# Kernel optimization log

Measured on AMD Instinct MI355X. Metric: run time of the kernel, lower is better.

The kernel has to match this reference:

```python
import jax, jax.numpy as jnp
from jax import lax
import numpy as np

SCALE = 1.0   # self.scale
EPS = 1e-12
CHUNK = 512   # points processed per chunk to bound [P,T,3] temporaries


def _closest_sqdist(p, a, b, c):
    """Squared distance from points p:[P,3] to triangles (a,b,c):[T,3] -> [P,T].
    Ericson's closest-point-on-triangle, fully vectorized."""
    ab = b - a
    ac = c - a
    bc = c - b
    ap = p[:, None, :] - a[None, :, :]
    bp = p[:, None, :] - b[None, :, :]
    cp = p[:, None, :] - c[None, :, :]
    d1 = jnp.einsum('td,ptd->pt', ab, ap)
    d2 = jnp.einsum('td,ptd->pt', ac, ap)
    d3 = jnp.einsum('td,ptd->pt', ab, bp)
    d4 = jnp.einsum('td,ptd->pt', ac, bp)
    d5 = jnp.einsum('td,ptd->pt', ab, cp)
    d6 = jnp.einsum('td,ptd->pt', ac, cp)
    va = d3 * d6 - d5 * d4
    vb = d5 * d2 - d1 * d6
    vc = d1 * d4 - d3 * d2

    def sdiv(n, d):  # NaN/Inf-safe division (branch is masked out by where anyway)
        return n / jnp.where(jnp.abs(d) < EPS, 1.0, d)

    t_ab = sdiv(d1, d1 - d3)[..., None]
    t_ac = sdiv(d2, d2 - d6)[..., None]
    t_bc = sdiv(d4 - d3, (d4 - d3) + (d5 - d6))[..., None]
    denom = va + vb + vc
    v_in = sdiv(vb, denom)[..., None]
    w_in = sdiv(vc, denom)[..., None]

    # base case: interior of the face; then overwrite with edge / vertex regions
    cl = a[None] + v_in * ab[None] + w_in * ac[None]
    cl = jnp.where(((va <= 0) & (d4 - d3 >= 0) & (d5 - d6 >= 0))[..., None],
                   b[None] + t_bc * bc[None], cl)   # edge BC
    cl = jnp.where(((vb <= 0) & (d2 >= 0) & (d6 <= 0))[..., None],
                   a[None] + t_ac * ac[None], cl)   # edge AC
    cl = jnp.where(((vc <= 0) & (d1 >= 0) & (d3 <= 0))[..., None],
                   a[None] + t_ab * ab[None], cl)   # edge AB
    cl = jnp.where(((d6 >= 0) & (d5 <= d6))[..., None], c[None], cl)  # vertex C
    cl = jnp.where(((d3 >= 0) & (d4 <= d3))[..., None], b[None], cl)  # vertex B
    cl = jnp.where(((d1 <= 0) & (d2 <= 0))[..., None], a[None], cl)   # vertex A
    diff = p[:, None, :] - cl
    return jnp.sum(diff * diff, axis=-1)


def setup_inputs():
    key = jax.random.key(0)
    k1, k2, k3 = jax.random.split(key, 3)
    vertices = jax.random.normal(k1, (4, 3, 16, 16, 16), dtype=jnp.float32)
    pc = jax.random.uniform(k2, (4, 4096, 3), dtype=jnp.float32)
    faces = jax.random.randint(k3, (8192, 3), 0, 4096, dtype=jnp.int32)
    return {"vertices": vertices, "pc": pc, "faces": faces}


def reference(vertices, pc, faces):
    B = vertices.shape[0]
    v = jax.nn.sigmoid(vertices)                     # self.normalization
    pos = jnp.moveaxis(v, 1, -1).reshape(B, -1, 3)   # permute(1,2,3,0).view(-1,3)
    pts = pc * SCALE                                 # _scale_points
    # pymesh path drops all-zero points; emulate with a mask (scaling keeps zeros zero)
    mask = jnp.any(pc != 0.0, axis=-1).astype(pts.dtype)  # [B,N]

    def per_batch(args):
        posb, pb, mb = args
        a = posb[faces[:, 0]]
        b = posb[faces[:, 1]]
        c = posb[faces[:, 2]]
        n_chunks = pb.shape[0] // CHUNK

        def chunk_min(pch):  # [CHUNK,3] -> [CHUNK] nearest sq-dist over all tris
            return jnp.min(_closest_sqdist(pch, a, b, c), axis=-1)

        d = lax.map(chunk_min, pb.reshape(n_chunks, CHUNK, 3)).reshape(-1)
        cnt = jnp.maximum(jnp.sum(mb), 1.0)
        return jnp.sum(d * mb) / cnt                 # mean(squared_distances)

    losses = lax.map(per_batch, (pos, pts, mask))    # [B]
    return jnp.mean(losses)
```

## Files before the change

### kernel.cpp

```cpp
#include <hip/hip_runtime.h>
#include <math.h>
#include <float.h>

#define NB 4
#define NP 4096
#define NT 8192
#define NS 64
#define TCH (NT/NS)
#define TREC 20
#define EPSD 1e-12

typedef float f2 __attribute__((ext_vector_type(2)));

__device__ __forceinline__ float sigm(float x) { return 1.0f / (1.0f + expf(-x)); }
__device__ __forceinline__ f2 vmin2(f2 a, f2 b) { return __builtin_elementwise_min(a, b); }
__device__ __forceinline__ f2 vmax2(f2 a, f2 b) { return __builtin_elementwise_max(a, b); }
__device__ __forceinline__ f2 clamp01(f2 x) {
  f2 z; z.x = 0.0f; z.y = 0.0f;
  f2 o; o.x = 1.0f; o.y = 1.0f;
  return vmin2(vmax2(x, z), o);
}

__global__ __launch_bounds__(256) void prep_kernel(
    const float* __restrict__ verts, const int* __restrict__ faces,
    float* __restrict__ tri)
{
  int idx = blockIdx.x * 256 + threadIdx.x;
  if (idx >= NB * NT) return;
  int b = idx >> 13;
  int t = idx & (NT - 1);
  int f0 = faces[3 * t + 0], f1 = faces[3 * t + 1], f2i = faces[3 * t + 2];
  const float* vb = verts + (size_t)b * 3 * NP;
  float ax = sigm(vb[f0]),  ay = sigm(vb[NP + f0]),  az = sigm(vb[2 * NP + f0]);
  float bx = sigm(vb[f1]),  by = sigm(vb[NP + f1]),  bz = sigm(vb[2 * NP + f1]);
  float cx = sigm(vb[f2i]), cy = sigm(vb[NP + f2i]), cz = sigm(vb[2 * NP + f2i]);
  float abx = bx - ax, aby = by - ay, abz = bz - az;
  float acx = cx - ax, acy = cy - ay, acz = cz - az;
  double aa = (double)abx * abx + (double)aby * aby + (double)abz * abz;
  double am = (double)abx * acx + (double)aby * acy + (double)abz * acz;
  double cc = (double)acx * acx + (double)acy * acy + (double)acz * acz;
  double den = aa * cc - am * am;
  double bb  = aa - 2.0 * am + cc;
  float raa  = (fabs(aa)  < EPSD) ? 1.0f : (float)(1.0 / aa);
  float rcc  = (fabs(cc)  < EPSD) ? 1.0f : (float)(1.0 / cc);
  float rbb  = (fabs(bb)  < EPSD) ? 1.0f : (float)(1.0 / bb);
  float rden = (fabs(den) < EPSD) ? 0.0f : (float)(1.0 / den);
  float* r = tri + (size_t)idx * TREC;
  r[0]  = ax;  r[1]  = ay;  r[2]  = az;
  r[3]  = abx; r[4]  = aby; r[5]  = abz;
  r[6]  = acx; r[7]  = acy; r[8]  = acz;
  r[9]  = (float)aa; r[10] = (float)am; r[11] = (float)cc;
  r[12] = raa; r[13] = rcc; r[14] = rbb; r[15] = rden;
  r[16] = (float)den; r[17] = (float)bb; r[18] = (float)(aa - am); r[19] = 0.0f;
}

__global__ __launch_bounds__(256) void dist_kernel(
    const float* __restrict__ tri, const float* __restrict__ pc,
    float* __restrict__ part)
{
  int bid  = blockIdx.x;
  int pblk = bid & 7;
  int s    = (bid >> 3) & (NS - 1);
  int b    = bid >> 9;
  int p0   = pblk * 512 + threadIdx.x;
  const float* pp0 = pc + ((size_t)b * NP + p0) * 3;
  const float* pp1 = pp0 + 256 * 3;
  f2 px, py, pz;
  px.x = pp0[0]; px.y = pp1[0];
  py.x = pp0[1]; py.y = pp1[1];
  pz.x = pp0[2]; pz.y = pp1[2];

  const float4* __restrict__ R =
      (const float4*)(tri + (size_t)(b * NT + s * TCH) * TREC);
  f2 mind; mind.x = FLT_MAX; mind.y = FLT_MAX;

  #pragma unroll 2
  for (int t = 0; t < TCH; ++t) {
    float4 r0 = R[0], r1 = R[1], r2 = R[2], r3 = R[3], r4 = R[4];
    R += 5;
    float abx = r0.w, aby = r1.x, abz = r1.y;
    float acx = r1.z, acy = r1.w, acz = r2.x;
    float aa = r2.y, am = r2.z, cc = r2.w;
    float raa = r3.x, rcc = r3.y, rbb = r3.z, rden = r3.w;
    float den = r4.x, bb = r4.y, k1 = r4.z;

    f2 apx = px - r0.x, apy = py - r0.y, apz = pz - r0.z;

    f2 d1   = apx * abx + apy * aby + apz * abz;
    f2 d2   = apx * acx + apy * acy + apz * acz;
    f2 apap = apx * apx + apy * apy + apz * apz;

    f2 vb = d1 * cc - d2 * am;
    f2 vc = d2 * aa - d1 * am;
    f2 va = den - vb - vc;

    f2 di = apap - (vb * d1 + vc * d2) * rden;

    f2 t2 = d1 + d1;
    f2 tab = clamp01(d1 * raa);
    f2 dAB = apap + tab * (tab * aa - t2);

    f2 t4 = d2 + d2;
    f2 tac = clamp01(d2 * rcc);
    f2 dAC = apap + tac * (tac * cc - t4);

    f2 e = d2 - d1 + k1;
    f2 tbc = clamp01(e * rbb);
    f2 distB = apap - t2 + aa;
    f2 dBC = distB + tbc * (tbc * bb - (e + e));

    f2 m3 = vmin2(vmin2(dAB, dAC), dBC);

    bool in0 = (vb.x >= 0.0f) & (vc.x >= 0.0f) & (va.x > 0.0f);
    bool in1 = (vb.y >= 0.0f) & (vc.y >= 0.0f) & (va.y > 0.0f);
    f2 dist;
    dist.x = in0 ? di.x : m3.x;
    dist.y = in1 ? di.y : m3.y;

    mind = vmin2(mind, dist);
  }
  float* dst = part + ((size_t)b * NS + s) * NP + p0;
  dst[0]   = fmaxf(mind.x, 0.0f);
  dst[256] = fmaxf(mind.y, 0.0f);
}

__global__ __launch_bounds__(256) void reduce_kernel(
    const float* __restrict__ part, const float* __restrict__ pc,
    float* __restrict__ bl2)
{
  int blk = blockIdx.x;
  int b = blk >> 4;
  int p = (blk & 15) * 256 + threadIdx.x;
  float m = FLT_MAX;
  #pragma unroll
  for (int s = 0; s < NS; ++s)
    m = fminf(m, part[((size_t)b * NS + s) * NP + p]);
  const float* pp = pc + ((size_t)b * NP + p) * 3;
  float x = pp[0], y = pp[1], z = pp[2];
  float msk = ((x != 0.0f) | (y != 0.0f) | (z != 0.0f)) ? 1.0f : 0.0f;
  float sdm = m * msk, sm = msk;
  for (int off = 32; off > 0; off >>= 1) {
    sdm += __shfl_down(sdm, off, 64);
    sm  += __shfl_down(sm,  off, 64);
  }
  __shared__ float s1[4], s2[4];
  int wave = threadIdx.x >> 6, lane = threadIdx.x & 63;
  if (lane == 0) { s1[wave] = sdm; s2[wave] = sm; }
  __syncthreads();
  if (threadIdx.x == 0) {
    bl2[2 * blk]     = s1[0] + s1[1] + s1[2] + s1[3];
    bl2[2 * blk + 1] = s2[0] + s2[1] + s2[2] + s2[3];
  }
}

__global__ void final_kernel(const float* __restrict__ bl2, float* __restrict__ out)
{
  if (threadIdx.x == 0 && blockIdx.x == 0) {
    float acc = 0.0f;
    for (int b = 0; b < NB; ++b) {
      float sdm = 0.0f, sm = 0.0f;
      for (int k = 0; k < 16; ++k) {
        sdm += bl2[2 * (b * 16 + k)];
        sm  += bl2[2 * (b * 16 + k) + 1];
      }
      acc += sdm / fmaxf(sm, 1.0f);
    }
    out[0] = 0.25f * acc;
  }
}

extern "C" void kernel_launch(void* const* d_in, const int* in_sizes, int n_in,
                              void* d_out, int out_size, void* d_ws, size_t ws_size,
                              hipStream_t stream) {
  const float* verts = (const float*)d_in[0];
  const float* pc    = (const float*)d_in[1];
  const int*   faces = (const int*)d_in[2];
  float* out = (float*)d_out;

  float* tri  = (float*)d_ws;
  float* part = tri  + (size_t)NB * NT * TREC;
  float* bl2  = part + (size_t)NB * NS * NP;

  prep_kernel<<<(NB * NT) / 256, 256, 0, stream>>>(verts, faces, tri);
  dist_kernel<<<NB * NS * 8, 256, 0, stream>>>(tri, pc, part);
  reduce_kernel<<<NB * 16, 256, 0, stream>>>(part, pc, bl2);
  final_kernel<<<1, 64, 0, stream>>>(bl2, out);
}
```

Measured before the change: 179.3 us.

## Cull triangles by plane distance with warm-start bound and wave-queued exact tests

Replaces the brute-force point-triangle distance loop with two passes. A warm pass computes exact distances against the first 512 triangles to get an upper bound per point. The main pass then culls each remaining triangle using the squared distance to its plane, with a slightly inflated denominator. Surviving (point, triangle) pairs go into a per-wave LDS queue and are evaluated in batches of 64, with atomicMin into shared per-point minima. This trades fewer full distance evaluations for ballot/queue overhead, divergence, and dependence on how effective the culling is for random triangles.

```diff
diff --git a/kernel.cpp b/kernel.cpp
--- a/kernel.cpp
+++ b/kernel.cpp
@@ -5,20 +5,46 @@
 #define NB 4
 #define NP 4096
 #define NT 8192
-#define NS 64
-#define TCH (NT/NS)
-#define TREC 20
+#define TREC 24
 #define EPSD 1e-12
-
-typedef float f2 __attribute__((ext_vector_type(2)));
+#define WNS 8
+#define WTCH 64
+#define WTOT (WNS*WTCH)
+#define MNS 16
+#define MTCH ((NT - WTOT)/MNS)
 
 __device__ __forceinline__ float sigm(float x) { return 1.0f / (1.0f + expf(-x)); }
-__device__ __forceinline__ f2 vmin2(f2 a, f2 b) { return __builtin_elementwise_min(a, b); }
-__device__ __forceinline__ f2 vmax2(f2 a, f2 b) { return __builtin_elementwise_max(a, b); }
-__device__ __forceinline__ f2 clamp01(f2 x) {
-  f2 z; z.x = 0.0f; z.y = 0.0f;
-  f2 o; o.x = 1.0f; o.y = 1.0f;
-  return vmin2(vmax2(x, z), o);
+
+__device__ __forceinline__ float tri_dist(
+    float px, float py, float pz,
+    float ax, float ay, float az,
+    float abx, float aby, float abz,
+    float acx, float acy, float acz,
+    float aa, float am, float cc,
+    float raa, float rcc, float rbb,
+    float rden, float den, float bb, float k1)
+{
+  float apx = px - ax, apy = py - ay, apz = pz - az;
+  float d1   = apx*abx + apy*aby + apz*abz;
+  float d2   = apx*acx + apy*acy + apz*acz;
+  float apap = apx*apx + apy*apy + apz*apz;
+  float vb = d1*cc - d2*am;
+  float vc = d2*aa - d1*am;
+  float va = den - vb - vc;
+  float di = apap - (vb*d1 + vc*d2)*rden;
+  float t2 = d1 + d1;
+  float tab = fminf(fmaxf(d1*raa, 0.0f), 1.0f);
+  float dAB = apap + tab*(tab*aa - t2);
+  float t4 = d2 + d2;
+  float tac = fminf(fmaxf(d2*rcc, 0.0f), 1.0f);
+  float dAC = apap + tac*(tac*cc - t4);
+  float e   = d2 - d1 + k1;
+  float tbc = fminf(fmaxf(e*rbb, 0.0f), 1.0f);
+  float distB = apap - t2 + aa;
+  float dBC = distB + tbc*(tbc*bb - (e + e));
+  float m3 = fminf(fminf(dAB, dAC), dBC);
+  bool in = (vb >= 0.0f) & (vc >= 0.0f) & (va > 0.0f);
+  return in ? di : m3;
 }
 
 __global__ __launch_bounds__(256) void prep_kernel(
@@ -29,99 +55,165 @@
   if (idx >= NB * NT) return;
   int b = idx >> 13;
   int t = idx & (NT - 1);
-  int f0 = faces[3 * t + 0], f1 = faces[3 * t + 1], f2i = faces[3 * t + 2];
-  const float* vb = verts + (size_t)b * 3 * NP;
-  float ax = sigm(vb[f0]),  ay = sigm(vb[NP + f0]),  az = sigm(vb[2 * NP + f0]);
-  float bx = sigm(vb[f1]),  by = sigm(vb[NP + f1]),  bz = sigm(vb[2 * NP + f1]);
-  float cx = sigm(vb[f2i]), cy = sigm(vb[NP + f2i]), cz = sigm(vb[2 * NP + f2i]);
+  int f0 = faces[3*t + 0], f1 = faces[3*t + 1], f2i = faces[3*t + 2];
+  const float* vb_ = verts + (size_t)b * 3 * NP;
+  float ax = sigm(vb_[f0]),  ay = sigm(vb_[NP + f0]),  az = sigm(vb_[2*NP + f0]);
+  float bx = sigm(vb_[f1]),  by = sigm(vb_[NP + f1]),  bz = sigm(vb_[2*NP + f1]);
+  float cx = sigm(vb_[f2i]), cy = sigm(vb_[NP + f2i]), cz = sigm(vb_[2*NP + f2i]);
   float abx = bx - ax, aby = by - ay, abz = bz - az;
   float acx = cx - ax, acy = cy - ay, acz = cz - az;
-  double aa = (double)abx * abx + (double)aby * aby + (double)abz * abz;
-  double am = (double)abx * acx + (double)aby * acy + (double)abz * acz;
-  double cc = (double)acx * acx + (double)acy * acy + (double)acz * acz;
-  double den = aa * cc - am * am;
-  double bb  = aa - 2.0 * am + cc;
-  float raa  = (fabs(aa)  < EPSD) ? 1.0f : (float)(1.0 / aa);
-  float rcc  = (fabs(cc)  < EPSD) ? 1.0f : (float)(1.0 / cc);
-  float rbb  = (fabs(bb)  < EPSD) ? 1.0f : (float)(1.0 / bb);
-  float rden = (fabs(den) < EPSD) ? 0.0f : (float)(1.0 / den);
+  double aa = (double)abx*abx + (double)aby*aby + (double)abz*abz;
+  double am = (double)abx*acx + (double)aby*acy + (double)abz*acz;
+  double cc = (double)acx*acx + (double)acy*acy + (double)acz*acz;
+  double den = aa*cc - am*am;
+  double bb  = aa - 2.0*am + cc;
+  float raa  = (fabs(aa)  < EPSD) ? 1.0f : (float)(1.0/aa);
+  float rcc  = (fabs(cc)  < EPSD) ? 1.0f : (float)(1.0/cc);
+  float rbb  = (fabs(bb)  < EPSD) ? 1.0f : (float)(1.0/bb);
+  float rden = (fabs(den) < EPSD) ? 0.0f : (float)(1.0/den);
+  double nx = (double)aby*acz - (double)abz*acy;
+  double ny = (double)abz*acx - (double)abx*acz;
+  double nz = (double)abx*acy - (double)aby*acx;
+  double na = nx*ax + ny*ay + nz*az;
+  float denadj = (fabs(den) < EPSD) ? 1e30f : (float)(den * 1.02);
   float* r = tri + (size_t)idx * TREC;
-  r[0]  = ax;  r[1]  = ay;  r[2]  = az;
-  r[3]  = abx; r[4]  = aby; r[5]  = abz;
-  r[6]  = acx; r[7]  = acy; r[8]  = acz;
-  r[9]  = (float)aa; r[10] = (float)am; r[11] = (float)cc;
-  r[12] = raa; r[13] = rcc; r[14] = rbb; r[15] = rden;
-  r[16] = (float)den; r[17] = (float)bb; r[18] = (float)(aa - am); r[19] = 0.0f;
-}
-
-__global__ __launch_bounds__(256) void dist_kernel(
+  r[0]  = (float)nx; r[1]  = (float)ny; r[2]  = (float)nz; r[3] = (float)(-na);
+  r[4]  = denadj;    r[5]  = ax;        r[6]  = ay;        r[7] = az;
+  r[8]  = abx;       r[9]  = aby;       r[10] = abz;       r[11] = acx;
+  r[12] = acy;       r[13] = acz;       r[14] = (float)aa; r[15] = (float)am;
+  r[16] = (float)cc; r[17] = raa;       r[18] = rcc;       r[19] = rbb;
+  r[20] = rden;      r[21] = (float)den;r[22] = (float)bb; r[23] = (float)(aa - am);
+}
+
+__global__ __launch_bounds__(256) void warm_kernel(
     const float* __restrict__ tri, const float* __restrict__ pc,
-    float* __restrict__ part)
+    float* __restrict__ partW)
 {
   int bid  = blockIdx.x;
-  int pblk = bid & 7;
-  int s    = (bid >> 3) & (NS - 1);
-  int b    = bid >> 9;
-  int p0   = pblk * 512 + threadIdx.x;
-  const float* pp0 = pc + ((size_t)b * NP + p0) * 3;
-  const float* pp1 = pp0 + 256 * 3;
-  f2 px, py, pz;
-  px.x = pp0[0]; px.y = pp1[0];
-  py.x = pp0[1]; py.y = pp1[1];
-  pz.x = pp0[2]; pz.y = pp1[2];
-
-  const float4* __restrict__ R =
-      (const float4*)(tri + (size_t)(b * NT + s * TCH) * TREC);
-  f2 mind; mind.x = FLT_MAX; mind.y = FLT_MAX;
-
-  #pragma unroll 2
-  for (int t = 0; t < TCH; ++t) {
-    float4 r0 = R[0], r1 = R[1], r2 = R[2], r3 = R[3], r4 = R[4];
-    R += 5;
-    float abx = r0.w, aby = r1.x, abz = r1.y;
-    float acx = r1.z, acy = r1.w, acz = r2.x;
-    float aa = r2.y, am = r2.z, cc = r2.w;
-    float raa = r3.x, rcc = r3.y, rbb = r3.z, rden = r3.w;
-    float den = r4.x, bb = r4.y, k1 = r4.z;
-
-    f2 apx = px - r0.x, apy = py - r0.y, apz = pz - r0.z;
-
-    f2 d1   = apx * abx + apy * aby + apz * abz;
-    f2 d2   = apx * acx + apy * acy + apz * acz;
-    f2 apap = apx * apx + apy * apy + apz * apz;
-
-    f2 vb = d1 * cc - d2 * am;
-    f2 vc = d2 * aa - d1 * am;
-    f2 va = den - vb - vc;
-
-    f2 di = apap - (vb * d1 + vc * d2) * rden;
-
-    f2 t2 = d1 + d1;
-    f2 tab = clamp01(d1 * raa);
-    f2 dAB = apap + tab * (tab * aa - t2);
-
-    f2 t4 = d2 + d2;
-    f2 tac = clamp01(d2 * rcc);
-    f2 dAC = apap + tac * (tac * cc - t4);
-
-    f2 e = d2 - d1 + k1;
-    f2 tbc = clamp01(e * rbb);
-    f2 distB = apap - t2 + aa;
-    f2 dBC = distB + tbc * (tbc * bb - (e + e));
-
-    f2 m3 = vmin2(vmin2(dAB, dAC), dBC);
-
-    bool in0 = (vb.x >= 0.0f) & (vc.x >= 0.0f) & (va.x > 0.0f);
-    bool in1 = (vb.y >= 0.0f) & (vc.y >= 0.0f) & (va.y > 0.0f);
-    f2 dist;
-    dist.x = in0 ? di.x : m3.x;
-    dist.y = in1 ? di.y : m3.y;
-
-    mind = vmin2(mind, dist);
-  }
-  float* dst = part + ((size_t)b * NS + s) * NP + p0;
-  dst[0]   = fmaxf(mind.x, 0.0f);
-  dst[256] = fmaxf(mind.y, 0.0f);
+  int pblk = bid & 15;
+  int s    = (bid >> 4) & (WNS - 1);
+  int b    = bid >> 7;
+  int p    = pblk * 256 + threadIdx.x;
+  const float* pp = pc + ((size_t)b * NP + p) * 3;
+  float px = pp[0], py = pp[1], pz = pp[2];
+  const float4* R = (const float4*)(tri + ((size_t)b * NT + s * WTCH) * TREC);
+  float mind = FLT_MAX;
+  float4 h1 = R[1], h2 = R[2], h3 = R[3], h4 = R[4], h5 = R[5];
+  for (int t = 0; t < WTCH; ++t) {
+    const float4* Rn = R + 6;
+    float4 g1 = Rn[1], g2 = Rn[2], g3 = Rn[3], g4 = Rn[4], g5 = Rn[5];
+    float dd = tri_dist(px, py, pz,
+                        h1.y, h1.z, h1.w,
+                        h2.x, h2.y, h2.z,
+                        h2.w, h3.x, h3.y,
+                        h3.z, h3.w, h4.x,
+                        h4.y, h4.z, h4.w,
+                        h5.x, h5.y, h5.z, h5.w);
+    mind = fminf(mind, dd);
+    h1 = g1; h2 = g2; h3 = g3; h4 = g4; h5 = g5;
+    R = Rn;
+  }
+  partW[((size_t)b * WNS + s) * NP + p] = fmaxf(mind, 0.0f);
+}
+
+__global__ __launch_bounds__(256) void main_kernel(
+    const float* __restrict__ tri, const float* __restrict__ pc,
+    const float* __restrict__ partW, float* __restrict__ partM)
+{
+  __shared__ unsigned qbuf[4][128];
+  __shared__ unsigned wmind[4][64];
+
+  int bid  = blockIdx.x;
+  int pblk = bid & 15;
+  int s    = (bid >> 4) & (MNS - 1);
+  int b    = bid >> 8;
+  int tid  = threadIdx.x;
+  int wave = tid >> 6, lane = tid & 63;
+  int p    = pblk * 256 + tid;
+
+  const float* pp = pc + ((size_t)b * NP + p) * 3;
+  float px = pp[0], py = pp[1], pz = pp[2];
+
+  float mind = FLT_MAX;
+  #pragma unroll
+  for (int j = 0; j < WNS; ++j)
+    mind = fminf(mind, partW[((size_t)b * WNS + j) * NP + p]);
+  wmind[wave][lane] = __float_as_uint(mind);
+
+  unsigned qcnt = 0u, qd = 0u;
+  const float* triB = tri + (size_t)b * NT * TREC;
+  int tg0 = WTOT + s * MTCH;
+  const float4* Rf = (const float4*)(triB + (size_t)tg0 * TREC);
+
+#define DRAIN_BATCH(NACT)                                                     \
+  {                                                                           \
+    unsigned ent = qbuf[wave][(qd + (unsigned)lane) & 127u];                  \
+    if ((unsigned)lane < (unsigned)(NACT)) {                                  \
+      int te  = (int)(ent >> 6);                                              \
+      int src = (int)(ent & 63u);                                             \
+      float qx = __shfl(px, src, 64);                                         \
+      float qy = __shfl(py, src, 64);                                         \
+      float qz = __shfl(pz, src, 64);                                         \
+      const float* rr = triB + (size_t)te * TREC;                             \
+      float4 w1 = *(const float4*)(rr + 4);                                   \
+      float4 w2 = *(const float4*)(rr + 8);                                   \
+      float4 w3 = *(const float4*)(rr + 12);                                  \
+      float4 w4 = *(const float4*)(rr + 16);                                  \
+      float4 w5 = *(const float4*)(rr + 20);                                  \
+      float dd = fmaxf(tri_dist(qx, qy, qz,                                   \
+                                w1.y, w1.z, w1.w,                             \
+                                w2.x, w2.y, w2.z,                             \
+                                w2.w, w3.x, w3.y,                             \
+                                w3.z, w3.w, w4.x,                             \
+                                w4.y, w4.z, w4.w,                             \
+                                w5.x, w5.y, w5.z, w5.w), 0.0f);               \
+      atomicMin(&wmind[wave][src], __float_as_uint(dd));                      \
+    }                                                                         \
+    qd += (unsigned)(NACT);                                                   \
+    mind = fminf(mind, __uint_as_float(wmind[wave][lane]));                   \
+  }
+
+#define SCAN_ITER(Q0, DA, TIDX)                                               \
+  {                                                                           \
+    float sN = fmaf(pz, (Q0).z, fmaf(py, (Q0).y, fmaf(px, (Q0).x, (Q0).w)));  \
+    bool pred = (sN * sN) < (mind * (DA));                                    \
+    unsigned long long mask = __ballot(pred);                                 \
+    if (mask) {                                                               \
+      if (pred) {                                                             \
+        int prefix = __builtin_amdgcn_mbcnt_hi((unsigned)(mask >> 32),        \
+                       __builtin_amdgcn_mbcnt_lo((unsigned)mask, 0));         \
+        qbuf[wave][(qcnt + (unsigned)prefix) & 127u] =                        \
+            ((unsigned)(TIDX) << 6) | (unsigned)lane;                         \
+      }                                                                       \
+      qcnt += (unsigned)__builtin_popcountll(mask);                           \
+      if (qcnt - qd >= 64u) DRAIN_BATCH(64u);                                 \
+    }                                                                         \
+  }
+
+  float4 c00 = Rf[0],  c01 = Rf[1],  c10 = Rf[6],  c11 = Rf[7];
+  float4 c20 = Rf[12], c21 = Rf[13], c30 = Rf[18], c31 = Rf[19];
+  int tg = tg0;
+  for (int g = 0; g < MTCH / 4; ++g) {
+    const float4* Rn = Rf + 24;
+    float4 n00 = Rn[0],  n01 = Rn[1],  n10 = Rn[6],  n11 = Rn[7];
+    float4 n20 = Rn[12], n21 = Rn[13], n30 = Rn[18], n31 = Rn[19];
+    SCAN_ITER(c00, c01.x, tg + 0);
+    SCAN_ITER(c10, c11.x, tg + 1);
+    SCAN_ITER(c20, c21.x, tg + 2);
+    SCAN_ITER(c30, c31.x, tg + 3);
+    c00 = n00; c01 = n01; c10 = n10; c11 = n11;
+    c20 = n20; c21 = n21; c30 = n30; c31 = n31;
+    Rf = Rn; tg += 4;
+  }
+
+  unsigned pend = qcnt - qd;
+  if (pend) DRAIN_BATCH(pend);
+  mind = fminf(mind, __uint_as_float(wmind[wave][lane]));
+
+  partM[((size_t)b * MNS + s) * NP + p] = fmaxf(mind, 0.0f);
+
+#undef SCAN_ITER
+#undef DRAIN_BATCH
 }
 
 __global__ __launch_bounds__(256) void reduce_kernel(
@@ -133,8 +225,8 @@
   int p = (blk & 15) * 256 + threadIdx.x;
   float m = FLT_MAX;
   #pragma unroll
-  for (int s = 0; s < NS; ++s)
-    m = fminf(m, part[((size_t)b * NS + s) * NP + p]);
+  for (int s = 0; s < MNS; ++s)
+    m = fminf(m, part[((size_t)b * MNS + s) * NP + p]);
   const float* pp = pc + ((size_t)b * NP + p) * 3;
   float x = pp[0], y = pp[1], z = pp[2];
   float msk = ((x != 0.0f) | (y != 0.0f) | (z != 0.0f)) ? 1.0f : 0.0f;
@@ -144,8 +236,8 @@
     sm  += __shfl_down(sm,  off, 64);
   }
   __shared__ float s1[4], s2[4];
-  int wave = threadIdx.x >> 6, lane = threadIdx.x & 63;
-  if (lane == 0) { s1[wave] = sdm; s2[wave] = sm; }
+  int wave = threadIdx.x >> 6, lanei = threadIdx.x & 63;
+  if (lanei == 0) { s1[wave] = sdm; s2[wave] = sm; }
   __syncthreads();
   if (threadIdx.x == 0) {
     bl2[2 * blk]     = s1[0] + s1[1] + s1[2] + s1[3];
@@ -177,12 +269,14 @@
   const int*   faces = (const int*)d_in[2];
   float* out = (float*)d_out;
 
-  float* tri  = (float*)d_ws;
-  float* part = tri  + (size_t)NB * NT * TREC;
-  float* bl2  = part + (size_t)NB * NS * NP;
+  float* tri   = (float*)d_ws;
+  float* partW = tri   + (size_t)NB * NT * TREC;
+  float* partM = partW + (size_t)NB * WNS * NP;
+  float* bl2   = partM + (size_t)NB * MNS * NP;
 
   prep_kernel<<<(NB * NT) / 256, 256, 0, stream>>>(verts, faces, tri);
-  dist_kernel<<<NB * NS * 8, 256, 0, stream>>>(tri, pc, part);
-  reduce_kernel<<<NB * 16, 256, 0, stream>>>(part, pc, bl2);
+  warm_kernel<<<NB * WNS * 16, 256, 0, stream>>>(tri, pc, partW);
+  main_kernel<<<NB * MNS * 16, 256, 0, stream>>>(tri, pc, partW, partM);
+  reduce_kernel<<<NB * 16, 256, 0, stream>>>(partM, pc, bl2);
   final_kernel<<<1, 64, 0, stream>>>(bl2, out);
 }
```

After: 170.4 us. 1.05x faster.
